# Kernel optimization log

Measured on AMD Instinct MI355X. Metric: run time of the kernel, lower is better.

The kernel has to match this reference:

```python
import jax, jax.numpy as jnp
import numpy as np

N_NODES = 50000
IN, H, OUT = 128, 256, 128  # in_channels, hidden_channels, out_channels
E, PE = 640000, 500000
EPS = 1e-5


def setup_inputs() -> dict:
    key = jax.random.key(0)
    ks = jax.random.split(key, 12)
    def rn(k, shape, s=0.05):
        return jax.random.normal(k, shape, jnp.float32) * s
    return {
        "x": jax.random.normal(ks[0], (N_NODES, IN), jnp.float32),
        "edge_index": jax.random.randint(ks[1], (2, E), 0, N_NODES, jnp.int32),
        "pred_edge_index": jax.random.randint(ks[2], (2, PE), 0, N_NODES, jnp.int32),
        # SAGEConv 1: out = mean_neighbors @ W_l^T + x @ W_r^T + b (PyG default, root_weight=True)
        "W1l": rn(ks[3], (H, IN)), "W1r": rn(ks[4], (H, IN)), "b1": jnp.zeros((H,), jnp.float32),
        "bn1_g": jnp.ones((H,), jnp.float32), "bn1_b": jnp.zeros((H,), jnp.float32),
        "bn1_m": jnp.zeros((H,), jnp.float32), "bn1_v": jnp.ones((H,), jnp.float32),
        # SAGEConv 2
        "W2l": rn(ks[5], (OUT, H)), "W2r": rn(ks[6], (OUT, H)), "b2": jnp.zeros((OUT,), jnp.float32),
        # LinkPredictor MLP
        "pW1": rn(ks[7], (H, 2 * OUT)), "pb1": jnp.zeros((H,), jnp.float32),
        "pbn1_g": jnp.ones((H,), jnp.float32), "pbn1_b": jnp.zeros((H,), jnp.float32),
        "pbn1_m": jnp.zeros((H,), jnp.float32), "pbn1_v": jnp.ones((H,), jnp.float32),
        "pW2": rn(ks[8], (H // 2, H)), "pb2": jnp.zeros((H // 2,), jnp.float32),
        "pbn2_g": jnp.ones((H // 2,), jnp.float32), "pbn2_b": jnp.zeros((H // 2,), jnp.float32),
        "pbn2_m": jnp.zeros((H // 2,), jnp.float32), "pbn2_v": jnp.ones((H // 2,), jnp.float32),
        "pW3": rn(ks[9], (1, H // 2)), "pb3": jnp.zeros((1,), jnp.float32),
    }


def _bn(x, g, b, m, v):
    # BatchNorm1d in eval mode (running stats)
    return (x - m) * jax.lax.rsqrt(v + EPS) * g + b


def _sage(x, src, dst, Wl, Wr, b):
    # mean aggregation of source features onto targets (gather-scatter)
    agg = jax.ops.segment_sum(x[src], dst, num_segments=N_NODES)
    cnt = jax.ops.segment_sum(jnp.ones(src.shape, x.dtype), dst, num_segments=N_NODES)
    mean = agg / jnp.maximum(cnt, 1.0)[:, None]
    return mean @ Wl.T + x @ Wr.T + b


def reference(x, edge_index, pred_edge_index, W1l, W1r, b1, bn1_g, bn1_b, bn1_m, bn1_v,
              W2l, W2r, b2, pW1, pb1, pbn1_g, pbn1_b, pbn1_m, pbn1_v,
              pW2, pb2, pbn2_g, pbn2_b, pbn2_m, pbn2_v, pW3, pb3):
    src, dst = edge_index[0], edge_index[1]
    # encoder (dropout is identity in eval mode)
    h = _sage(x, src, dst, W1l, W1r, b1)
    h = jax.nn.relu(_bn(h, bn1_g, bn1_b, bn1_m, bn1_v))
    z = _sage(h, src, dst, W2l, W2r, b2)  # [N_NODES, OUT]
    # decoder: gather endpoint embeddings and run MLP
    q = jnp.concatenate([z[pred_edge_index[0]], z[pred_edge_index[1]]], axis=-1)  # [PE, 2*OUT]
    q = jax.nn.relu(_bn(q @ pW1.T + pb1, pbn1_g, pbn1_b, pbn1_m, pbn1_v))
    q = jax.nn.relu(_bn(q @ pW2.T + pb2, pbn2_g, pbn2_b, pbn2_m, pbn2_v))
    return (q @ pW3.T + pb3).squeeze(-1)  # [PE]
```

## Files before the change

kernel.cpp:

```cpp
#include <hip/hip_runtime.h>
#include <hip/hip_bf16.h>

#define NN   50000
#define NE   640000
#define NPE  500000
#define FEPS 1e-5f

typedef __attribute__((ext_vector_type(8))) short          bf16x8;
typedef __attribute__((ext_vector_type(8))) unsigned short u16x8;
typedef __attribute__((ext_vector_type(4))) float          f32x4;

__device__ inline float b2f(unsigned short u) {
    union { unsigned int i; float f; } c; c.i = (unsigned int)u << 16; return c.f;
}
__device__ inline unsigned short f2b(float f) {
    __hip_bfloat16 h = __float2bfloat16(f);
    return *reinterpret_cast<unsigned short*>(&h);
}

__global__ __launch_bounds__(256) void k_init(
    int4* __restrict__ zdst,
    const float* __restrict__ x, unsigned short* __restrict__ xbf,
    const float* __restrict__ W1l, const float* __restrict__ W1r,
    const float* __restrict__ W2l, const float* __restrict__ W2r,
    const float* __restrict__ pW1, const float* __restrict__ pW2,
    unsigned short* __restrict__ wdst) {
    int b = blockIdx.x, t = threadIdx.x;
    if (b < 98) {
        int i = b * 256 + t;
        if (i < 25088) zdst[i] = make_int4(0, 0, 0, 0);
        return;
    }
    const float* src;
    unsigned short* dst;
    size_t off;
    if (b < 3223) {
        int i = (b - 98) * 256 + t;
        if (i >= 800000) return;
        src = x; dst = xbf; off = i;
        const float4* p = (const float4*)src + 2 * off;
        float4 a = p[0], c = p[1];
        u16x8 o;
        o[0]=f2b(a.x); o[1]=f2b(a.y); o[2]=f2b(a.z); o[3]=f2b(a.w);
        o[4]=f2b(c.x); o[5]=f2b(c.y); o[6]=f2b(c.z); o[7]=f2b(c.w);
        *((u16x8*)dst + off) = o;
        return;
    }
    int i = (b - 3223) * 256 + t;
    if (i >= 28672) return;
    if      (i < 4096)  { src = W1l; off = i; }
    else if (i < 8192)  { src = W1r; off = i - 4096; }
    else if (i < 12288) { src = W2l; off = i - 8192; }
    else if (i < 16384) { src = W2r; off = i - 12288; }
    else if (i < 24576) { src = pW1; off = i - 16384; }
    else                { src = pW2; off = i - 24576; }
    const float4* p = (const float4*)src + 2 * off;
    float4 a = p[0], c = p[1];
    u16x8 o;
    o[0]=f2b(a.x); o[1]=f2b(a.y); o[2]=f2b(a.z); o[3]=f2b(a.w);
    o[4]=f2b(c.x); o[5]=f2b(c.y); o[6]=f2b(c.z); o[7]=f2b(c.w);
    *((u16x8*)wdst + i) = o;
}

__global__ void k_hist(const int* __restrict__ dst, int* __restrict__ cnt) {
    int e = blockIdx.x * blockDim.x + threadIdx.x;
    if (e < NE) atomicAdd(&cnt[dst[e]], 1);
}

__global__ void k_scan1(const int* __restrict__ cnt, int* __restrict__ part) {
    int t = threadIdx.x, lane = t & 63, w = t >> 6;
    int i = blockIdx.x * 256 + t;
    int v = (i < NN) ? cnt[i] : 0;
#pragma unroll
    for (int d = 1; d < 64; d <<= 1) v += __shfl_xor(v, d, 64);
    __shared__ int ws[4];
    if (lane == 0) ws[w] = v;
    __syncthreads();
    if (t == 0) part[blockIdx.x] = ws[0] + ws[1] + ws[2] + ws[3];
}

__global__ void k_scan2(int* __restrict__ part) {
    int t = threadIdx.x, lane = t & 63, w = t >> 6;
    int v = (t < 196) ? part[t] : 0;
    int s = v;
#pragma unroll
    for (int d = 1; d < 64; d <<= 1) { int u = __shfl_up(s, d, 64); if (lane >= d) s += u; }
    __shared__ int ws[4];
    if (lane == 63) ws[w] = s;
    __syncthreads();
    if (t == 0) { int a = 0; for (int k = 0; k < 4; ++k) { int tmp = ws[k]; ws[k] = a; a += tmp; } }
    __syncthreads();
    if (t < 196) part[t] = ws[w] + s - v;
}

__global__ void k_scan3(const int* __restrict__ cnt, const int* __restrict__ part,
                        int* __restrict__ rowptr) {
    int t = threadIdx.x, lane = t & 63, w = t >> 6;
    int i = blockIdx.x * 256 + t;
    int v = (i < NN) ? cnt[i] : 0;
    int s = v;
#pragma unroll
    for (int d = 1; d < 64; d <<= 1) { int u = __shfl_up(s, d, 64); if (lane >= d) s += u; }
    __shared__ int ws[4];
    if (lane == 63) ws[w] = s;
    __syncthreads();
    if (t == 0) { int a = 0; for (int k = 0; k < 4; ++k) { int tmp = ws[k]; ws[k] = a; a += tmp; } }
    __syncthreads();
    if (i <= NN) rowptr[i] = part[blockIdx.x] + ws[w] + s - v;
}

__global__ void k_fill(const int* __restrict__ src, const int* __restrict__ dst,
                       const int* __restrict__ rowptr, int* __restrict__ cursor,
                       int* __restrict__ col) {
    int e = blockIdx.x * blockDim.x + threadIdx.x;
    if (e >= NE) return;
    int d = dst[e];
    int slot = atomicAdd(&cursor[d], 1);
    col[rowptr[d] + slot] = src[e];
}

__global__ __launch_bounds__(256) void k_mean(const unsigned short* __restrict__ feat,
                                              const int* __restrict__ rowptr,
                                              const int* __restrict__ col,
                                              unsigned short* __restrict__ outm) {
    int node = blockIdx.x * 4 + (threadIdx.x >> 6);
    int lane = threadIdx.x & 63;
    if (node >= NN) return;
    int beg = rowptr[node], end = rowptr[node + 1];
    float a0 = 0.f, a1 = 0.f;
    int j = beg;
    for (; j + 8 <= end; j += 8) {
        int s[8];
#pragma unroll
        for (int k = 0; k < 8; ++k) s[k] = col[j + k];
        unsigned int v[8];
#pragma unroll
        for (int k = 0; k < 8; ++k)
            v[k] = *(const unsigned int*)(feat + (size_t)s[k] * 128 + lane * 2);
#pragma unroll
        for (int k = 0; k < 8; ++k) { a0 += b2f(v[k] & 0xffff); a1 += b2f(v[k] >> 16); }
    }
    if (j + 4 <= end) {
        int s[4];
#pragma unroll
        for (int k = 0; k < 4; ++k) s[k] = col[j + k];
        unsigned int v[4];
#pragma unroll
        for (int k = 0; k < 4; ++k)
            v[k] = *(const unsigned int*)(feat + (size_t)s[k] * 128 + lane * 2);
#pragma unroll
        for (int k = 0; k < 4; ++k) { a0 += b2f(v[k] & 0xffff); a1 += b2f(v[k] >> 16); }
        j += 4;
    }
    for (; j < end; ++j) {
        int s = col[j];
        unsigned int v = *(const unsigned int*)(feat + (size_t)s * 128 + lane * 2);
        a0 += b2f(v & 0xffff); a1 += b2f(v >> 16);
    }
    float inv = 1.f / fmaxf((float)(end - beg), 1.f);
    unsigned int v = (unsigned int)f2b(a0 * inv) | ((unsigned int)f2b(a1 * inv) << 16);
    *(unsigned int*)(outm + (size_t)node * 128 + lane * 2) = v;
}

__global__ __launch_bounds__(256) void k_sage1(
    const unsigned short* __restrict__ mean, const unsigned short* __restrict__ self,
    const unsigned short* __restrict__ Wl, const unsigned short* __restrict__ Wr,
    const float* __restrict__ b, const float* __restrict__ bg, const float* __restrict__ bb,
    const float* __restrict__ bm, const float* __restrict__ bv,
    unsigned short* __restrict__ hout) {
    __shared__ unsigned short ms[64 * 128];
    __shared__ unsigned short xs[64 * 128];
    int t = threadIdx.x;
    int n0 = blockIdx.x * 64;
    for (int j = 0; j < 4; ++j) {
        int idx = t + j * 256;
        int row = idx >> 4, c16 = idx & 15;
        int node = n0 + row;
        u16x8 v = {0,0,0,0,0,0,0,0}, v2 = {0,0,0,0,0,0,0,0};
        if (node < NN) {
            v  = *(const u16x8*)(mean + (size_t)node * 128 + c16 * 8);
            v2 = *(const u16x8*)(self + (size_t)node * 128 + c16 * 8);
        }
        int byte = row * 256 + ((c16 * 16) ^ ((row & 7) << 4));
        *(u16x8*)((char*)ms + byte) = v;
        *(u16x8*)((char*)xs + byte) = v2;
    }
    __syncthreads();
    int w = t >> 6, l = t & 63, lr = l & 15, lh = l >> 4;
    f32x4 acc[4][4];
#pragma unroll
    for (int mi = 0; mi < 4; ++mi)
#pragma unroll
        for (int ni = 0; ni < 4; ++ni) { acc[mi][ni][0]=0; acc[mi][ni][1]=0; acc[mi][ni][2]=0; acc[mi][ni][3]=0; }
#pragma unroll
    for (int half = 0; half < 2; ++half) {
        const unsigned short* A = half ? xs : ms;
        const unsigned short* W = half ? Wr : Wl;
#pragma unroll
        for (int ks = 0; ks < 4; ++ks) {
            int k0 = ks * 32;
            bf16x8 a[4], wf[4];
#pragma unroll
            for (int mi = 0; mi < 4; ++mi) {
                int row = mi * 16 + lr;
                int byte = row * 256 + ((k0 * 2 + lh * 16) ^ ((row & 7) << 4));
                a[mi] = *(const bf16x8*)((const char*)A + byte);
            }
#pragma unroll
            for (int ni = 0; ni < 4; ++ni) {
                int wrow = w * 64 + ni * 16 + lr;
                wf[ni] = *(const bf16x8*)(W + (size_t)wrow * 128 + k0 + lh * 8);
            }
#pragma unroll
            for (int mi = 0; mi < 4; ++mi)
#pragma unroll
                for (int ni = 0; ni < 4; ++ni)
                    acc[mi][ni] = __builtin_amdgcn_mfma_f32_16x16x32_bf16(a[mi], wf[ni], acc[mi][ni], 0, 0, 0);
        }
    }
#pragma unroll
    for (int ni = 0; ni < 4; ++ni) {
        int ch = w * 64 + ni * 16 + lr;
        float sc = bg[ch] * rsqrtf(bv[ch] + FEPS);
        float sh = bb[ch] - bm[ch] * sc;
        float bias = b[ch];
#pragma unroll
        for (int mi = 0; mi < 4; ++mi)
#pragma unroll
            for (int r = 0; r < 4; ++r) {
                int node = n0 + mi * 16 + lh * 4 + r;
                if (node < NN) {
                    float vv = (acc[mi][ni][r] + bias) * sc + sh;
                    hout[(size_t)node * 256 + ch] = f2b(fmaxf(vv, 0.f));
                }
            }
    }
}

__global__ __launch_bounds__(256) void k_lin2(
    const unsigned short* __restrict__ h,
    const unsigned short* __restrict__ Wl,
    const unsigned short* __restrict__ Wr,
    const float* __restrict__ b2,
    unsigned short* __restrict__ Y, unsigned short* __restrict__ S) {
    __shared__ unsigned short hs[64 * 256];
    int t = threadIdx.x;
    int n0 = blockIdx.x * 64;
    for (int j = 0; j < 8; ++j) {
        int idx = t + j * 256;
        int row = idx >> 5, c16 = idx & 31;
        int node = n0 + row;
        u16x8 v = {0,0,0,0,0,0,0,0};
        if (node < NN) v = *(const u16x8*)(h + (size_t)node * 256 + c16 * 8);
        int byte = row * 512 + ((c16 * 16) ^ ((row & 7) << 4));
        *(u16x8*)((char*)hs + byte) = v;
    }
    __syncthreads();
    int w = t >> 6, l = t & 63, lr = l & 15, lh = l >> 4;
    f32x4 aY[4][2], aS[4][2];
#pragma unroll
    for (int mi = 0; mi < 4; ++mi)
#pragma unroll
        for (int ni = 0; ni < 2; ++ni) {
            aY[mi][ni][0]=0; aY[mi][ni][1]=0; aY[mi][ni][2]=0; aY[mi][ni][3]=0;
            aS[mi][ni][0]=0; aS[mi][ni][1]=0; aS[mi][ni][2]=0; aS[mi][ni][3]=0;
        }
#pragma unroll
    for (int ks = 0; ks < 8; ++ks) {
        int k0 = ks * 32;
        bf16x8 a[4], wl[2], wr[2];
#pragma unroll
        for (int mi = 0; mi < 4; ++mi) {
            int row = mi * 16 + lr;
            int byte = row * 512 + ((k0 * 2 + lh * 16) ^ ((row & 7) << 4));
            a[mi] = *(const bf16x8*)((const char*)hs + byte);
        }
#pragma unroll
        for (int ni = 0; ni < 2; ++ni) {
            int wrow = w * 32 + ni * 16 + lr;
            wl[ni] = *(const bf16x8*)(Wl + (size_t)wrow * 256 + k0 + lh * 8);
            wr[ni] = *(const bf16x8*)(Wr + (size_t)wrow * 256 + k0 + lh * 8);
        }
#pragma unroll
        for (int mi = 0; mi < 4; ++mi)
#pragma unroll
            for (int ni = 0; ni < 2; ++ni) {
                aY[mi][ni] = __builtin_amdgcn_mfma_f32_16x16x32_bf16(a[mi], wl[ni], aY[mi][ni], 0, 0, 0);
                aS[mi][ni] = __builtin_amdgcn_mfma_f32_16x16x32_bf16(a[mi], wr[ni], aS[mi][ni], 0, 0, 0);
            }
    }
#pragma unroll
    for (int ni = 0; ni < 2; ++ni) {
        int ch = w * 32 + ni * 16 + lr;
        float bias = b2[ch];
#pragma unroll
        for (int mi = 0; mi < 4; ++mi)
#pragma unroll
            for (int r = 0; r < 4; ++r) {
                int node = n0 + mi * 16 + lh * 4 + r;
                if (node < NN) {
                    Y[(size_t)node * 128 + ch] = f2b(aY[mi][ni][r]);
                    S[(size_t)node * 128 + ch] = f2b(aS[mi][ni][r] + bias);
                }
            }
    }
}

__global__ __launch_bounds__(256) void k_prep(
    const unsigned short* __restrict__ S,
    const unsigned short* __restrict__ mY,
    const unsigned short* __restrict__ W1,
    const float* __restrict__ b1, const float* __restrict__ g1,
    const float* __restrict__ be1, const float* __restrict__ m1, const float* __restrict__ v1,
    unsigned short* __restrict__ Pa, unsigned short* __restrict__ Pb) {
    __shared__ unsigned short zs[64 * 128];
    int t = threadIdx.x;
    int tile = blockIdx.x >> 1, side = blockIdx.x & 1;
    int n0 = tile * 64;
    for (int j = 0; j < 4; ++j) {
        int idx = t + j * 256;
        int row = idx >> 4, c16 = idx & 15;
        int node = n0 + row;
        u16x8 o = {0,0,0,0,0,0,0,0};
        if (node < NN) {
            u16x8 sv = *(const u16x8*)(S  + (size_t)node * 128 + c16 * 8);
            u16x8 mv = *(const u16x8*)(mY + (size_t)node * 128 + c16 * 8);
#pragma unroll
            for (int jj = 0; jj < 8; ++jj)
                o[jj] = f2b(b2f((unsigned short)sv[jj]) + b2f((unsigned short)mv[jj]));
        }
        int byte = row * 256 + ((c16 * 16) ^ ((row & 7) << 4));
        *(u16x8*)((char*)zs + byte) = o;
    }
    __syncthreads();
    int w = t >> 6, l = t & 63, lr = l & 15, lh = l >> 4;
    f32x4 acc[4][4];
#pragma unroll
    for (int mi = 0; mi < 4; ++mi)
#pragma unroll
        for (int ni = 0; ni < 4; ++ni) { acc[mi][ni][0]=0; acc[mi][ni][1]=0; acc[mi][ni][2]=0; acc[mi][ni][3]=0; }
#pragma unroll
    for (int ks = 0; ks < 4; ++ks) {
        int k0 = ks * 32;
        bf16x8 a[4], wf[4];
#pragma unroll
        for (int mi = 0; mi < 4; ++mi) {
            int row = mi * 16 + lr;
            int byte = row * 256 + ((k0 * 2 + lh * 16) ^ ((row & 7) << 4));
            a[mi] = *(const bf16x8*)((const char*)zs + byte);
        }
#pragma unroll
        for (int ni = 0; ni < 4; ++ni) {
            int ch = w * 64 + ni * 16 + lr;
            wf[ni] = *(const bf16x8*)(W1 + (size_t)ch * 256 + side * 128 + k0 + lh * 8);
        }
#pragma unroll
        for (int mi = 0; mi < 4; ++mi)
#pragma unroll
            for (int ni = 0; ni < 4; ++ni)
                acc[mi][ni] = __builtin_amdgcn_mfma_f32_16x16x32_bf16(a[mi], wf[ni], acc[mi][ni], 0, 0, 0);
    }
    unsigned short* P = side ? Pb : Pa;
#pragma unroll
    for (int ni = 0; ni < 4; ++ni) {
        int ch = w * 64 + ni * 16 + lr;
        float sc = g1[ch] * rsqrtf(v1[ch] + FEPS);
        float add = side ? 0.f : ((b1[ch] - m1[ch]) * sc + be1[ch]);
#pragma unroll
        for (int mi = 0; mi < 4; ++mi)
#pragma unroll
            for (int r = 0; r < 4; ++r) {
                int node = n0 + mi * 16 + lh * 4 + r;
                if (node < NN)
                    P[(size_t)node * 256 + ch] = f2b(acc[mi][ni][r] * sc + add);
            }
    }
}

__global__ __launch_bounds__(256, 5) void k_mlp(
    const unsigned short* __restrict__ Pa, const unsigned short* __restrict__ Pb,
    const int* __restrict__ pu, const int* __restrict__ pv,
    const unsigned short* __restrict__ W2, const float* __restrict__ b2,
    const float* __restrict__ g2, const float* __restrict__ be2,
    const float* __restrict__ m2, const float* __restrict__ v2,
    const float* __restrict__ W3, const float* __restrict__ b3,
    float* __restrict__ out) {
    __shared__ unsigned short q1[64 * 256];
    int t = threadIdx.x;
    int e0 = blockIdx.x * 64;
#pragma unroll
    for (int batch = 0; batch < 2; ++batch) {
        u16x8 A[4], B[4];
        int bofs[4];
#pragma unroll
        for (int j = 0; j < 4; ++j) {
            int idx = t + (batch * 4 + j) * 256;
            int edge = idx >> 5, c16 = idx & 31;
            int ge = e0 + edge;
            if (ge < NPE) {
                int u = pu[ge], vv = pv[ge];
                A[j] = *(const u16x8*)(Pa + (size_t)u  * 256 + c16 * 8);
                B[j] = *(const u16x8*)(Pb + (size_t)vv * 256 + c16 * 8);
            } else {
                A[j] = (u16x8){0,0,0,0,0,0,0,0};
                B[j] = (u16x8){0,0,0,0,0,0,0,0};
            }
            bofs[j] = edge * 512 + ((c16 * 16) ^ ((edge & 7) << 4));
        }
#pragma unroll
        for (int j = 0; j < 4; ++j) {
            u16x8 o;
#pragma unroll
            for (int jj = 0; jj < 8; ++jj)
                o[jj] = f2b(fmaxf(b2f((unsigned short)A[j][jj]) + b2f((unsigned short)B[j][jj]), 0.f));
            *(u16x8*)((char*)q1 + bofs[j]) = o;
        }
    }
    __syncthreads();
    int w = t >> 6, l = t & 63, lr = l & 15, lh = l >> 4;
    f32x4 acc[4][2];
#pragma unroll
    for (int mi = 0; mi < 4; ++mi)
#pragma unroll
        for (int ni = 0; ni < 2; ++ni) { acc[mi][ni][0]=0; acc[mi][ni][1]=0; acc[mi][ni][2]=0; acc[mi][ni][3]=0; }
#pragma unroll
    for (int ks = 0; ks < 8; ++ks) {
        int k0 = ks * 32;
        bf16x8 a[4], wf[2];
#pragma unroll
        for (int mi = 0; mi < 4; ++mi) {
            int row = mi * 16 + lr;
            int byte = row * 512 + ((k0 * 2 + lh * 16) ^ ((row & 7) << 4));
            a[mi] = *(const bf16x8*)((const char*)q1 + byte);
        }
#pragma unroll
        for (int ni = 0; ni < 2; ++ni) {
            int wrow = w * 32 + ni * 16 + lr;
            wf[ni] = *(const bf16x8*)(W2 + (size_t)wrow * 256 + k0 + lh * 8);
        }
#pragma unroll
        for (int mi = 0; mi < 4; ++mi)
#pragma unroll
            for (int ni = 0; ni < 2; ++ni)
                acc[mi][ni] = __builtin_amdgcn_mfma_f32_16x16x32_bf16(a[mi], wf[ni], acc[mi][ni], 0, 0, 0);
    }
    __syncthreads();
#pragma unroll
    for (int ni = 0; ni < 2; ++ni) {
        int ch = w * 32 + ni * 16 + lr;
        float sc = g2[ch] * rsqrtf(v2[ch] + FEPS);
        float sh = be2[ch] - m2[ch] * sc;
        float bias = b2[ch];
#pragma unroll
        for (int mi = 0; mi < 4; ++mi)
#pragma unroll
            for (int r = 0; r < 4; ++r) {
                int row = mi * 16 + lh * 4 + r;
                float vv = fmaxf((acc[mi][ni][r] + bias) * sc + sh, 0.f);
                int byte = row * 256 + ((ch * 2) ^ ((row & 7) << 4));
                *(unsigned short*)((char*)q1 + byte) = f2b(vv);
            }
    }
    __syncthreads();
    {
        int edge = t >> 2, part = t & 3;
        float p = 0.f;
#pragma unroll
        for (int s = 0; s < 4; ++s) {
            int byte = edge * 256 + ((part * 64 + s * 16) ^ ((edge & 7) << 4));
            u16x8 v = *(const u16x8*)((const char*)q1 + byte);
#pragma unroll
            for (int jj = 0; jj < 8; ++jj)
                p += b2f((unsigned short)v[jj]) * W3[part * 32 + s * 8 + jj];
        }
        p += __shfl_xor(p, 1, 64);
        p += __shfl_xor(p, 2, 64);
        int ge = e0 + edge;
        if (part == 0 && ge < NPE) out[ge] = p + b3[0];
    }
}

extern "C" void kernel_launch(void* const* d_in, const int* in_sizes, int n_in,
                              void* d_out, int out_size, void* d_ws, size_t ws_size,
                              hipStream_t stream) {
    const float* x    = (const float*)d_in[0];
    const int*   ei   = (const int*)d_in[1];
    const int*   pei  = (const int*)d_in[2];
    const float* W1l  = (const float*)d_in[3];
    const float* W1r  = (const float*)d_in[4];
    const float* b1   = (const float*)d_in[5];
    const float* bn1g = (const float*)d_in[6];
    const float* bn1b = (const float*)d_in[7];
    const float* bn1m = (const float*)d_in[8];
    const float* bn1v = (const float*)d_in[9];
    const float* W2l  = (const float*)d_in[10];
    const float* W2r  = (const float*)d_in[11];
    const float* b2   = (const float*)d_in[12];
    const float* pW1  = (const float*)d_in[13];
    const float* pb1  = (const float*)d_in[14];
    const float* pg1  = (const float*)d_in[15];
    const float* pbb1 = (const float*)d_in[16];
    const float* pm1  = (const float*)d_in[17];
    const float* pv1  = (const float*)d_in[18];
    const float* pW2  = (const float*)d_in[19];
    const float* pb2  = (const float*)d_in[20];
    const float* pg2  = (const float*)d_in[21];
    const float* pbb2 = (const float*)d_in[22];
    const float* pm2  = (const float*)d_in[23];
    const float* pv2  = (const float*)d_in[24];
    const float* pW3  = (const float*)d_in[25];
    const float* pb3  = (const float*)d_in[26];
    float* out = (float*)d_out;

    const int* src = ei;
    const int* dst = ei + NE;
    const int* pu  = pei;
    const int* pv  = pei + NPE;

    char* p = (char*)d_ws;
    auto alloc = [&](size_t bytes) -> char* {
        char* r = p; p += (bytes + 255) & ~(size_t)255; return r;
    };
    int* cnt    = (int*)alloc((size_t)NN * 4);
    int* cursor = (int*)alloc((size_t)NN * 4);
    int* part   = (int*)alloc(256 * 4);
    int* rowptr = (int*)alloc((size_t)(NN + 1) * 4);
    int* col    = (int*)alloc((size_t)NE * 4);
    unsigned short* xbf  = (unsigned short*)alloc((size_t)NN * 128 * 2);
    unsigned short* mx   = (unsigned short*)alloc((size_t)NN * 128 * 2);
    unsigned short* hbf  = (unsigned short*)alloc((size_t)NN * 256 * 2);
    unsigned short* Ybf  = (unsigned short*)alloc((size_t)NN * 128 * 2);
    unsigned short* mY   = (unsigned short*)alloc((size_t)NN * 128 * 2);
    unsigned short* Sbf  = (unsigned short*)alloc((size_t)NN * 128 * 2);
    unsigned short* W1lb = (unsigned short*)alloc((size_t)256 * 128 * 2);
    unsigned short* W1rb = (unsigned short*)alloc((size_t)256 * 128 * 2);
    unsigned short* W2lb = (unsigned short*)alloc((size_t)128 * 256 * 2);
    unsigned short* W2rb = (unsigned short*)alloc((size_t)128 * 256 * 2);
    unsigned short* pW1b = (unsigned short*)alloc((size_t)256 * 256 * 2);
    unsigned short* pW2b = (unsigned short*)alloc((size_t)128 * 256 * 2);
    unsigned short* Pa = hbf;
    unsigned short* Pb = xbf;

    k_init<<<3335, 256, 0, stream>>>((int4*)cnt, x, xbf,
                                     W1l, W1r, W2l, W2r, pW1, pW2, W1lb);
    k_hist<<<2500, 256, 0, stream>>>(dst, cnt);
    k_scan1<<<196, 256, 0, stream>>>(cnt, part);
    k_scan2<<<1, 256, 0, stream>>>(part);
    k_scan3<<<196, 256, 0, stream>>>(cnt, part, rowptr);
    k_fill<<<2500, 256, 0, stream>>>(src, dst, rowptr, cursor, col);

    k_mean<<<12500, 256, 0, stream>>>(xbf, rowptr, col, mx);
    k_sage1<<<782, 256, 0, stream>>>(mx, xbf, W1lb, W1rb, b1, bn1g, bn1b, bn1m, bn1v, hbf);
    k_lin2<<<782, 256, 0, stream>>>(hbf, W2lb, W2rb, b2, Ybf, Sbf);
    k_mean<<<12500, 256, 0, stream>>>(Ybf, rowptr, col, mY);

    k_prep<<<1564, 256, 0, stream>>>(Sbf, mY, pW1b, pb1, pg1, pbb1, pm1, pv1, Pa, Pb);

    k_mlp<<<(NPE + 63) / 64, 256, 0, stream>>>(Pa, Pb, pu, pv,
                                               pW2b, pb2, pg2, pbb2, pm2, pv2,
                                               pW3, pb3, out);
}
```

Before: 374.9 us.

## Fuse SAGE layers, sort prediction edges by source, remap MLP blocks per XCD

```diff
diff --git a/kernel.cpp b/kernel.cpp
--- a/kernel.cpp
+++ b/kernel.cpp
@@ -26,27 +26,25 @@
     const float* __restrict__ pW1, const float* __restrict__ pW2,
     unsigned short* __restrict__ wdst) {
     int b = blockIdx.x, t = threadIdx.x;
-    if (b < 98) {
+    if (b < 196) {
         int i = b * 256 + t;
-        if (i < 25088) zdst[i] = make_int4(0, 0, 0, 0);
+        if (i < 50048) zdst[i] = make_int4(0, 0, 0, 0);
         return;
     }
     const float* src;
-    unsigned short* dst;
     size_t off;
-    if (b < 3223) {
-        int i = (b - 98) * 256 + t;
+    if (b < 3321) {
+        int i = (b - 196) * 256 + t;
         if (i >= 800000) return;
-        src = x; dst = xbf; off = i;
-        const float4* p = (const float4*)src + 2 * off;
+        const float4* p = (const float4*)x + 2 * (size_t)i;
         float4 a = p[0], c = p[1];
         u16x8 o;
         o[0]=f2b(a.x); o[1]=f2b(a.y); o[2]=f2b(a.z); o[3]=f2b(a.w);
         o[4]=f2b(c.x); o[5]=f2b(c.y); o[6]=f2b(c.z); o[7]=f2b(c.w);
-        *((u16x8*)dst + off) = o;
+        *((u16x8*)xbf + i) = o;
         return;
     }
-    int i = (b - 3223) * 256 + t;
+    int i = (b - 3321) * 256 + t;
     if (i >= 28672) return;
     if      (i < 4096)  { src = W1l; off = i; }
     else if (i < 8192)  { src = W1r; off = i - 4096; }
@@ -62,9 +60,9 @@
     *((u16x8*)wdst + i) = o;
 }
 
-__global__ void k_hist(const int* __restrict__ dst, int* __restrict__ cnt) {
+__global__ void k_hist(const int* __restrict__ key, int* __restrict__ cnt, int n) {
     int e = blockIdx.x * blockDim.x + threadIdx.x;
-    if (e < NE) atomicAdd(&cnt[dst[e]], 1);
+    if (e < n) atomicAdd(&cnt[key[e]], 1);
 }
 
 __global__ void k_scan1(const int* __restrict__ cnt, int* __restrict__ part) {
@@ -117,6 +115,18 @@
     int d = dst[e];
     int slot = atomicAdd(&cursor[d], 1);
     col[rowptr[d] + slot] = src[e];
+}
+
+__global__ void k_fill2(const int* __restrict__ pu, const int* __restrict__ pv,
+                        const int* __restrict__ rowptr2, int* __restrict__ cursor2,
+                        int* __restrict__ su, int2* __restrict__ svi) {
+    int e = blockIdx.x * blockDim.x + threadIdx.x;
+    if (e >= NPE) return;
+    int u = pu[e];
+    int slot = atomicAdd(&cursor2[u], 1);
+    int pos = rowptr2[u] + slot;
+    su[pos] = u;
+    svi[pos] = make_int2(pv[e], e);
 }
 
 __global__ __launch_bounds__(256) void k_mean(const unsigned short* __restrict__ feat,
@@ -162,14 +172,17 @@
     *(unsigned int*)(outm + (size_t)node * 128 + lane * 2) = v;
 }
 
-__global__ __launch_bounds__(256) void k_sage1(
+__global__ __launch_bounds__(256) void k_sage12(
     const unsigned short* __restrict__ mean, const unsigned short* __restrict__ self,
     const unsigned short* __restrict__ Wl, const unsigned short* __restrict__ Wr,
     const float* __restrict__ b, const float* __restrict__ bg, const float* __restrict__ bb,
     const float* __restrict__ bm, const float* __restrict__ bv,
-    unsigned short* __restrict__ hout) {
-    __shared__ unsigned short ms[64 * 128];
-    __shared__ unsigned short xs[64 * 128];
+    const unsigned short* __restrict__ W2l, const unsigned short* __restrict__ W2r,
+    const float* __restrict__ b2,
+    unsigned short* __restrict__ Y, unsigned short* __restrict__ S) {
+    __shared__ unsigned short AB[64 * 256];
+    unsigned short* ms = AB;
+    unsigned short* xs = AB + 64 * 128;
     int t = threadIdx.x;
     int n0 = blockIdx.x * 64;
     for (int j = 0; j < 4; ++j) {
@@ -218,6 +231,7 @@
                     acc[mi][ni] = __builtin_amdgcn_mfma_f32_16x16x32_bf16(a[mi], wf[ni], acc[mi][ni], 0, 0, 0);
         }
     }
+    __syncthreads();
 #pragma unroll
     for (int ni = 0; ni < 4; ++ni) {
         int ch = w * 64 + ni * 16 + lr;
@@ -228,35 +242,13 @@
         for (int mi = 0; mi < 4; ++mi)
 #pragma unroll
             for (int r = 0; r < 4; ++r) {
-                int node = n0 + mi * 16 + lh * 4 + r;
-                if (node < NN) {
-                    float vv = (acc[mi][ni][r] + bias) * sc + sh;
-                    hout[(size_t)node * 256 + ch] = f2b(fmaxf(vv, 0.f));
-                }
-            }
-    }
-}
-
-__global__ __launch_bounds__(256) void k_lin2(
-    const unsigned short* __restrict__ h,
-    const unsigned short* __restrict__ Wl,
-    const unsigned short* __restrict__ Wr,
-    const float* __restrict__ b2,
-    unsigned short* __restrict__ Y, unsigned short* __restrict__ S) {
-    __shared__ unsigned short hs[64 * 256];
-    int t = threadIdx.x;
-    int n0 = blockIdx.x * 64;
-    for (int j = 0; j < 8; ++j) {
-        int idx = t + j * 256;
-        int row = idx >> 5, c16 = idx & 31;
-        int node = n0 + row;
-        u16x8 v = {0,0,0,0,0,0,0,0};
-        if (node < NN) v = *(const u16x8*)(h + (size_t)node * 256 + c16 * 8);
-        int byte = row * 512 + ((c16 * 16) ^ ((row & 7) << 4));
-        *(u16x8*)((char*)hs + byte) = v;
-    }
-    __syncthreads();
-    int w = t >> 6, l = t & 63, lr = l & 15, lh = l >> 4;
+                int row = mi * 16 + lh * 4 + r;
+                float vv = fmaxf((acc[mi][ni][r] + bias) * sc + sh, 0.f);
+                int byte = row * 512 + ((ch * 2) ^ ((row & 7) << 4));
+                *(unsigned short*)((char*)AB + byte) = f2b(vv);
+            }
+    }
+    __syncthreads();
     f32x4 aY[4][2], aS[4][2];
 #pragma unroll
     for (int mi = 0; mi < 4; ++mi)
@@ -273,13 +265,13 @@
         for (int mi = 0; mi < 4; ++mi) {
             int row = mi * 16 + lr;
             int byte = row * 512 + ((k0 * 2 + lh * 16) ^ ((row & 7) << 4));
-            a[mi] = *(const bf16x8*)((const char*)hs + byte);
+            a[mi] = *(const bf16x8*)((const char*)AB + byte);
         }
 #pragma unroll
         for (int ni = 0; ni < 2; ++ni) {
             int wrow = w * 32 + ni * 16 + lr;
-            wl[ni] = *(const bf16x8*)(Wl + (size_t)wrow * 256 + k0 + lh * 8);
-            wr[ni] = *(const bf16x8*)(Wr + (size_t)wrow * 256 + k0 + lh * 8);
+            wl[ni] = *(const bf16x8*)(W2l + (size_t)wrow * 256 + k0 + lh * 8);
+            wr[ni] = *(const bf16x8*)(W2r + (size_t)wrow * 256 + k0 + lh * 8);
         }
 #pragma unroll
         for (int mi = 0; mi < 4; ++mi)
@@ -379,7 +371,7 @@
 
 __global__ __launch_bounds__(256, 5) void k_mlp(
     const unsigned short* __restrict__ Pa, const unsigned short* __restrict__ Pb,
-    const int* __restrict__ pu, const int* __restrict__ pv,
+    const int* __restrict__ su, const int2* __restrict__ svi,
     const unsigned short* __restrict__ W2, const float* __restrict__ b2,
     const float* __restrict__ g2, const float* __restrict__ be2,
     const float* __restrict__ m2, const float* __restrict__ v2,
@@ -387,7 +379,11 @@
     float* __restrict__ out) {
     __shared__ unsigned short q1[64 * 256];
     int t = threadIdx.x;
-    int e0 = blockIdx.x * 64;
+    const int q = 976, r = 5;
+    int bid = blockIdx.x;
+    int xcd = bid & 7, ii = bid >> 3;
+    int wg = (xcd < r) ? (xcd * (q + 1) + ii) : (r * (q + 1) + (xcd - r) * q + ii);
+    int e0 = wg * 64;
 #pragma unroll
     for (int batch = 0; batch < 2; ++batch) {
         u16x8 A[4], B[4];
@@ -398,9 +394,10 @@
             int edge = idx >> 5, c16 = idx & 31;
             int ge = e0 + edge;
             if (ge < NPE) {
-                int u = pu[ge], vv = pv[ge];
-                A[j] = *(const u16x8*)(Pa + (size_t)u  * 256 + c16 * 8);
-                B[j] = *(const u16x8*)(Pb + (size_t)vv * 256 + c16 * 8);
+                int u = su[ge];
+                int2 vi = svi[ge];
+                A[j] = *(const u16x8*)(Pa + (size_t)u    * 256 + c16 * 8);
+                B[j] = *(const u16x8*)(Pb + (size_t)vi.x * 256 + c16 * 8);
             } else {
                 A[j] = (u16x8){0,0,0,0,0,0,0,0};
                 B[j] = (u16x8){0,0,0,0,0,0,0,0};
@@ -476,7 +473,7 @@
         p += __shfl_xor(p, 1, 64);
         p += __shfl_xor(p, 2, 64);
         int ge = e0 + edge;
-        if (part == 0 && ge < NPE) out[ge] = p + b3[0];
+        if (part == 0 && ge < NPE) out[svi[ge].y] = p + b3[0];
     }
 }
 
@@ -521,42 +518,52 @@
     auto alloc = [&](size_t bytes) -> char* {
         char* r = p; p += (bytes + 255) & ~(size_t)255; return r;
     };
-    int* cnt    = (int*)alloc((size_t)NN * 4);
-    int* cursor = (int*)alloc((size_t)NN * 4);
-    int* part   = (int*)alloc(256 * 4);
-    int* rowptr = (int*)alloc((size_t)(NN + 1) * 4);
-    int* col    = (int*)alloc((size_t)NE * 4);
+    int* cnt     = (int*)alloc((size_t)NN * 4);
+    int* cursor  = (int*)alloc((size_t)NN * 4);
+    int* cnt2    = (int*)alloc((size_t)NN * 4);
+    int* cursor2 = (int*)alloc((size_t)NN * 4);
+    int* part    = (int*)alloc(256 * 4);
+    int* part2   = (int*)alloc(256 * 4);
+    int* rowptr  = (int*)alloc((size_t)(NN + 1) * 4);
+    int* rowptr2 = (int*)alloc((size_t)(NN + 1) * 4);
+    int* col     = (int*)alloc((size_t)NE * 4);
+    int* su      = (int*)alloc((size_t)NPE * 4);
+    int2* svi    = (int2*)alloc((size_t)NPE * 8);
     unsigned short* xbf  = (unsigned short*)alloc((size_t)NN * 128 * 2);
     unsigned short* mx   = (unsigned short*)alloc((size_t)NN * 128 * 2);
-    unsigned short* hbf  = (unsigned short*)alloc((size_t)NN * 256 * 2);
     unsigned short* Ybf  = (unsigned short*)alloc((size_t)NN * 128 * 2);
     unsigned short* mY   = (unsigned short*)alloc((size_t)NN * 128 * 2);
     unsigned short* Sbf  = (unsigned short*)alloc((size_t)NN * 128 * 2);
+    unsigned short* Pa   = (unsigned short*)alloc((size_t)NN * 256 * 2);
     unsigned short* W1lb = (unsigned short*)alloc((size_t)256 * 128 * 2);
     unsigned short* W1rb = (unsigned short*)alloc((size_t)256 * 128 * 2);
     unsigned short* W2lb = (unsigned short*)alloc((size_t)128 * 256 * 2);
     unsigned short* W2rb = (unsigned short*)alloc((size_t)128 * 256 * 2);
     unsigned short* pW1b = (unsigned short*)alloc((size_t)256 * 256 * 2);
     unsigned short* pW2b = (unsigned short*)alloc((size_t)128 * 256 * 2);
-    unsigned short* Pa = hbf;
     unsigned short* Pb = xbf;
 
-    k_init<<<3335, 256, 0, stream>>>((int4*)cnt, x, xbf,
+    k_init<<<3433, 256, 0, stream>>>((int4*)cnt, x, xbf,
                                      W1l, W1r, W2l, W2r, pW1, pW2, W1lb);
-    k_hist<<<2500, 256, 0, stream>>>(dst, cnt);
+    k_hist<<<2500, 256, 0, stream>>>(dst, cnt, NE);
     k_scan1<<<196, 256, 0, stream>>>(cnt, part);
     k_scan2<<<1, 256, 0, stream>>>(part);
     k_scan3<<<196, 256, 0, stream>>>(cnt, part, rowptr);
     k_fill<<<2500, 256, 0, stream>>>(src, dst, rowptr, cursor, col);
+    k_hist<<<1954, 256, 0, stream>>>(pu, cnt2, NPE);
+    k_scan1<<<196, 256, 0, stream>>>(cnt2, part2);
+    k_scan2<<<1, 256, 0, stream>>>(part2);
+    k_scan3<<<196, 256, 0, stream>>>(cnt2, part2, rowptr2);
+    k_fill2<<<1954, 256, 0, stream>>>(pu, pv, rowptr2, cursor2, su, svi);
 
     k_mean<<<12500, 256, 0, stream>>>(xbf, rowptr, col, mx);
-    k_sage1<<<782, 256, 0, stream>>>(mx, xbf, W1lb, W1rb, b1, bn1g, bn1b, bn1m, bn1v, hbf);
-    k_lin2<<<782, 256, 0, stream>>>(hbf, W2lb, W2rb, b2, Ybf, Sbf);
+    k_sage12<<<782, 256, 0, stream>>>(mx, xbf, W1lb, W1rb, b1, bn1g, bn1b, bn1m, bn1v,
+                                      W2lb, W2rb, b2, Ybf, Sbf);
     k_mean<<<12500, 256, 0, stream>>>(Ybf, rowptr, col, mY);
 
     k_prep<<<1564, 256, 0, stream>>>(Sbf, mY, pW1b, pb1, pg1, pbb1, pm1, pv1, Pa, Pb);
 
-    k_mlp<<<(NPE + 63) / 64, 256, 0, stream>>>(Pa, Pb, pu, pv,
+    k_mlp<<<(NPE + 63) / 64, 256, 0, stream>>>(Pa, Pb, su, svi,
                                                pW2b, pb2, pg2, pbb2, pm2, pv2,
                                                pW3, pb3, out);
 }
```

Measured after the change: 418.1 us. 1.12x slower.
